# Kernel optimization log

Hardware: AMD Instinct MI355X
Metric: run time of the kernel (lower is better)

The kernel has to match this reference:

```python
import jax, jax.numpy as jnp
import numpy as np

NUM_EMB = 1024
EMB_DIM = 256
COMM_COST = 0.25
BETA = 0.25


def setup_inputs() -> dict:
    key = jax.random.key(0)
    k1, k2 = jax.random.split(key)
    x = jax.random.normal(k1, (16, EMB_DIM, 64, 64), dtype=jnp.float32)
    # nn.Embedding initialized uniform(-1/num_emb, 1/num_emb)
    emb_weight = jax.random.uniform(
        k2, (NUM_EMB, EMB_DIM), dtype=jnp.float32,
        minval=-1.0 / NUM_EMB, maxval=1.0 / NUM_EMB)
    return {"x": x, "emb_weight": emb_weight}


def reference(x, emb_weight):
    # x: [B, C, H, W] -> [B, H, W, C]
    xp = jnp.transpose(x, (0, 2, 3, 1))
    B, H, W, C = xp.shape
    flat = xp.reshape(-1, C)  # [N, C]
    # squared euclidean distances (argmin-equivalent to torch.cdist)
    d2 = (jnp.sum(flat * flat, axis=1, keepdims=True)
          - 2.0 * jnp.einsum('nc,kc->nk', flat, emb_weight)
          + jnp.sum(emb_weight * emb_weight, axis=1))  # [N, K]
    idx = jnp.argmin(d2, axis=1)  # [N]
    quantized = emb_weight[idx].reshape(B, H, W, C)
    e_latent_loss = jnp.mean((jax.lax.stop_gradient(quantized) - xp) ** 2) * BETA
    q_latent_loss = jnp.mean((quantized - jax.lax.stop_gradient(xp)) ** 2)
    c_loss = q_latent_loss + COMM_COST * e_latent_loss
    # straight-through estimator
    quant_st = xp + jax.lax.stop_gradient(quantized - xp)
    quant_out = jnp.transpose(quant_st, (0, 3, 1, 2))  # [B, C, H, W]
    return (c_loss, quant_out)
```

## Files before the change

kernel.cpp:

```cpp
#include <hip/hip_runtime.h>
#include <hip/hip_bf16.h>
#include <cstdint>
#include <cstddef>

#define EMB_K   1024
#define EMB_C   256
#define HWB     4096
#define NPIX    65536

typedef __bf16 bf16x8 __attribute__((ext_vector_type(8)));
typedef float  f32x4  __attribute__((ext_vector_type(4)));

__device__ __forceinline__ unsigned short bf16bits(float v) {
  __hip_bfloat16 h = __float2bfloat16(v);
  return __builtin_bit_cast(unsigned short, h);
}

__global__ void k_emb(const float* __restrict__ emb, unsigned short* __restrict__ emb_bf,
                      float* __restrict__ enorm, float* __restrict__ loss,
                      unsigned* __restrict__ ctr) {
  int k = blockIdx.x;
  int c = threadIdx.x;
  if (k == 0 && c == 0) { *loss = 0.f; *ctr = 0u; }
  float v = emb[(size_t)k * EMB_C + c];
  emb_bf[(size_t)k * EMB_C + c] = bf16bits(v);
  float s = v * v;
  for (int m = 32; m; m >>= 1) s += __shfl_down(s, m, 64);
  __shared__ float red[4];
  int lane = c & 63, w = c >> 6;
  if (lane == 0) red[w] = s;
  __syncthreads();
  if (c == 0) enorm[k] = red[0] + red[1] + red[2] + red[3];
}

__device__ __forceinline__ void stage64(const unsigned short* __restrict__ rows,
                                        unsigned char* buf, int t) {
#pragma unroll
  for (int j = 0; j < 4; ++j) {
    int d = j * 512 + t;
    int r = d >> 5;
    int slot = d & 31;
    int c16 = ((slot >> 3) << 3) | ((slot & 7) ^ (r & 7));
    const unsigned short* src = rows + (size_t)r * EMB_C + c16 * 8;
    __builtin_amdgcn_global_load_lds(
        (const __attribute__((address_space(1))) void*)src,
        (__attribute__((address_space(3))) void*)(buf + (unsigned)(j * 8192 + (t >> 6) * 1024)),
        16, 0, 0);
  }
}

__device__ __forceinline__ int posA(int cc, int nl) {
  return ((cc >> 3) << 3) | ((cc & 7) ^ ((nl ^ (nl >> 2)) & 7));
}

#define LDS_BYTES 137280

__global__ __launch_bounds__(512) void
k_main(const float* __restrict__ x, const float* __restrict__ emb,
       const unsigned short* __restrict__ embbf, const float* __restrict__ enorm,
       float* __restrict__ out, float* __restrict__ loss, unsigned* __restrict__ ctr) {
  extern __shared__ char smem[];
  unsigned char* Abase = (unsigned char*)smem + 65536;
  float*    cjl    = (float*)(smem + 131072);
  unsigned* keys_l = (unsigned*)(smem + 135168);
  float*    xn_l   = (float*)(smem + 136192);
  float*    red    = (float*)(smem + 137216);

  int n0 = blockIdx.x * 256;
  int b  = n0 >> 12, hw0 = n0 & 4095;
  int t = threadIdx.x, w = t >> 6, lane = t & 63;
  int quad = lane >> 4, lr = lane & 15;
  int g  = w >> 1;
  int h2 = w & 1;

  stage64(embbf,               (unsigned char*)smem,         t);
  stage64(embbf + 64 * EMB_C,  (unsigned char*)smem + 32768, t);

  if (t < 256) { keys_l[t] = 0u; xn_l[t] = 0.f; }
  for (int i = t; i < 1024; i += 512) cjl[i] = 0.375f - 0.5f * enorm[i];
  __syncthreads();

  bf16x8 af[4][8];
#pragma unroll
  for (int p = 0; p < 2; ++p) {
    if (p) __syncthreads();
    {
      int hwq = t & 31;
      int cg  = t >> 5;
      const float* xp = x + (size_t)b * (EMB_C * HWB) + hw0 + p * 128 + hwq * 4;
      float xn[4] = {0.f, 0.f, 0.f, 0.f};
      unsigned pk[4][8] = {};
#pragma unroll
      for (int j = 0; j < 16; ++j) {
        f32x4 v = *(const f32x4*)(xp + (size_t)(cg * 16 + j) * HWB);
#pragma unroll
        for (int m = 0; m < 4; ++m) {
          xn[m] += v[m] * v[m];
          pk[m][j >> 1] |= (unsigned)bf16bits(v[m]) << ((j & 1) * 16);
        }
      }
#pragma unroll
      for (int m = 0; m < 4; ++m) {
        int nl = hwq * 4 + m;
        *(uint4*)(Abase + nl * 512 + posA(cg * 2,     nl) * 16) = *(const uint4*)&pk[m][0];
        *(uint4*)(Abase + nl * 512 + posA(cg * 2 + 1, nl) * 16) = *(const uint4*)&pk[m][4];
        atomicAdd(&xn_l[p * 128 + nl], xn[m]);
      }
    }
    __syncthreads();
    if ((g >> 1) == p) {
#pragma unroll
      for (int i = 0; i < 4; ++i) {
        int rA = (g & 1) * 64 + i * 16 + lr;
#pragma unroll
        for (int s = 0; s < 8; ++s) {
          int cc = s * 4 + quad;
          af[i][s] = *(const bf16x8*)(Abase + rA * 512 + posA(cc, rA) * 16);
        }
      }
    }
  }
  __syncthreads();

  unsigned best[4][4] = {};
  for (int kt = 0; kt < 16; ++kt) {
    if (kt < 14)
      stage64(embbf + (size_t)(kt + 2) * 64 * EMB_C,
              (unsigned char*)smem + (((kt + 2) & 3) << 15), t);
    if (kt < 14)       asm volatile("s_waitcnt vmcnt(8)" ::: "memory");
    else if (kt == 14) asm volatile("s_waitcnt vmcnt(4)" ::: "memory");
    else               asm volatile("s_waitcnt vmcnt(0)" ::: "memory");
    __builtin_amdgcn_s_barrier();
    __builtin_amdgcn_sched_barrier(0);
    const unsigned char* srcB = (const unsigned char*)smem + ((kt & 3) << 15);
    float cj[2]; unsigned kp[2];
#pragma unroll
    for (int j = 0; j < 2; ++j) {
      int k = kt * 64 + h2 * 32 + j * 16 + lr;
      cj[j] = cjl[k];
      kp[j] = 1023u - (unsigned)k;
    }
    f32x4 acc[4][2] = {};
#pragma unroll
    for (int s = 0; s < 8; ++s) {
      int cc = s * 4 + quad;
      int pos = ((cc >> 3) << 3) | ((cc & 7) ^ (lr & 7));
      bf16x8 bf[2];
#pragma unroll
      for (int j = 0; j < 2; ++j)
        bf[j] = *(const bf16x8*)(srcB + (h2 * 32 + j * 16 + lr) * 512 + pos * 16);
#pragma unroll
      for (int i = 0; i < 4; ++i)
#pragma unroll
        for (int j = 0; j < 2; ++j)
          acc[i][j] = __builtin_amdgcn_mfma_f32_16x16x32_bf16(af[i][s], bf[j], acc[i][j], 0, 0, 0);
    }
#pragma unroll
    for (int i = 0; i < 4; ++i)
#pragma unroll
      for (int j = 0; j < 2; ++j)
#pragma unroll
        for (int r = 0; r < 4; ++r) {
          float f = acc[i][j][r] + cj[j];
          unsigned key = (__float_as_uint(f) & 0xFFFFFC00u) | kp[j];
          best[i][r] = best[i][r] > key ? best[i][r] : key;
        }
  }
  __syncthreads();

#pragma unroll
  for (int i = 0; i < 4; ++i)
#pragma unroll
    for (int r = 0; r < 4; ++r) {
      unsigned v = best[i][r];
#pragma unroll
      for (int m = 1; m < 16; m <<= 1) {
        unsigned o = (unsigned)__shfl_xor((int)v, m, 64);
        v = v > o ? v : o;
      }
      if (lr == 0) atomicMax(&keys_l[g * 64 + i * 16 + quad * 4 + r], v);
    }
  __syncthreads();

  if (t < 256) {
    unsigned key = keys_l[t];
    float fh = __uint_as_float(key & 0xFFFFFC00u);
    float lsum = xn_l[t] + 0.75f - 2.0f * fh;
    for (int m = 32; m; m >>= 1) lsum += __shfl_down(lsum, m, 64);
    if (lane == 0) red[w] = lsum;
  }
  __syncthreads();
  if (t == 0) {
    atomicAdd(loss, red[0] + red[1] + red[2] + red[3]);
    __threadfence();
  }

  float* tile = (float*)smem;
  int nn = t >> 1, ch = t & 1;
  int idx = 1023 - (int)(keys_l[nn] & 1023u);
  const float* er = emb + (size_t)idx * EMB_C;
  int nrot = (nn - 3) & 255;
  float* ob = out + 1 + (size_t)b * (EMB_C * HWB) + hw0;
  for (int p = 0; p < 4; ++p) {
    int c0 = p * 64;
    if (p) __syncthreads();
#pragma unroll
    for (int q = 0; q < 8; ++q) {
      f32x4 v = *(const f32x4*)(er + c0 + ch * 32 + q * 4);
#pragma unroll
      for (int m = 0; m < 4; ++m)
        tile[(ch * 32 + q * 4 + m) * 256 + nrot] = v[m];
    }
    __syncthreads();
#pragma unroll
    for (int cc = 0; cc < 8; ++cc) {
      int cl = w * 8 + cc;
      const float* tr = tile + cl * 256;
      float* F = ob + (size_t)(c0 + cl) * HWB;
      if (lane < 63) {
        f32x4 q = *(const f32x4*)(tr + 4 * lane);
        *(f32x4*)(F + 3 + 4 * lane) = q;
      }
      if (lane == 0) { F[0] = tr[253]; F[1] = tr[254]; F[2] = tr[255]; }
      if (lane == 63) { F[255] = tr[252]; }
    }
  }

  if (t == 0) {
    unsigned done = atomicAdd(ctr, 1u);
    if (done == gridDim.x - 1) {
      float total = atomicAdd(loss, 0.f);
      out[0] = 1.0625f * total / 16777216.0f;
    }
  }
}

extern "C" void kernel_launch(void* const* d_in, const int* in_sizes, int n_in,
                              void* d_out, int out_size, void* d_ws, size_t ws_size,
                              hipStream_t stream) {
  const float* x   = (const float*)d_in[0];
  const float* emb = (const float*)d_in[1];
  float* out = (float*)d_out;
  char*  ws  = (char*)d_ws;

  unsigned short* emb_bf = (unsigned short*)ws;
  float*          enorm  = (float*)(ws + 524288);
  float*          loss   = (float*)(ws + 528384);
  unsigned*       ctr    = (unsigned*)(ws + 528388);

  hipFuncSetAttribute((const void*)k_main,
                      hipFuncAttributeMaxDynamicSharedMemorySize, LDS_BYTES);

  k_emb <<<dim3(EMB_K),      dim3(EMB_C), 0,         stream>>>(emb, emb_bf, enorm, loss, ctr);
  k_main<<<dim3(NPIX / 256), dim3(512),   LDS_BYTES, stream>>>(x, emb, emb_bf, enorm,
                                                               out, loss, ctr);
}
```

Baseline: 159.4 us.

## Load A fragments directly from global, reshape wave tiling, deepen B prefetch

Each wave now reads its 32 pixels' x values straight from global memory into MFMA A fragments, dropping the LDS transpose round trip, the xn atomics and several barriers. Every wave covers all 64 codes per k-tile on a 32-pixel slice instead of 64 pixels by 32 codes, so the per-pixel argmin no longer needs shared-memory atomicMax. The embedding prefetch becomes three tiles deep and is issued after the barrier. The output gather handles 128 channels per pass with two pixel rows per thread. The trade-off is strided scalar global loads for x in place of coalesced float4 reads, and a different register and LDS balance.

Result: no change. 161.6 us (+1.4%).

```diff
diff --git a/kernel.cpp b/kernel.cpp
--- a/kernel.cpp
+++ b/kernel.cpp
@@ -49,10 +49,6 @@
   }
 }
 
-__device__ __forceinline__ int posA(int cc, int nl) {
-  return ((cc >> 3) << 3) | ((cc & 7) ^ ((nl ^ (nl >> 2)) & 7));
-}
-
 #define LDS_BYTES 137280
 
 __global__ __launch_bounds__(512) void
@@ -60,7 +56,6 @@
        const unsigned short* __restrict__ embbf, const float* __restrict__ enorm,
        float* __restrict__ out, float* __restrict__ loss, unsigned* __restrict__ ctr) {
   extern __shared__ char smem[];
-  unsigned char* Abase = (unsigned char*)smem + 65536;
   float*    cjl    = (float*)(smem + 131072);
   unsigned* keys_l = (unsigned*)(smem + 135168);
   float*    xn_l   = (float*)(smem + 136192);
@@ -70,95 +65,87 @@
   int b  = n0 >> 12, hw0 = n0 & 4095;
   int t = threadIdx.x, w = t >> 6, lane = t & 63;
   int quad = lane >> 4, lr = lane & 15;
-  int g  = w >> 1;
-  int h2 = w & 1;
-
-  stage64(embbf,               (unsigned char*)smem,         t);
-  stage64(embbf + 64 * EMB_C,  (unsigned char*)smem + 32768, t);
-
-  if (t < 256) { keys_l[t] = 0u; xn_l[t] = 0.f; }
+
+  stage64(embbf,                (unsigned char*)smem,          t);
+  stage64(embbf + 64 * EMB_C,   (unsigned char*)smem + 32768,  t);
+  stage64(embbf + 128 * EMB_C,  (unsigned char*)smem + 65536,  t);
+
   for (int i = t; i < 1024; i += 512) cjl[i] = 0.375f - 0.5f * enorm[i];
-  __syncthreads();
-
-  bf16x8 af[4][8];
-#pragma unroll
-  for (int p = 0; p < 2; ++p) {
-    if (p) __syncthreads();
-    {
-      int hwq = t & 31;
-      int cg  = t >> 5;
-      const float* xp = x + (size_t)b * (EMB_C * HWB) + hw0 + p * 128 + hwq * 4;
-      float xn[4] = {0.f, 0.f, 0.f, 0.f};
-      unsigned pk[4][8] = {};
-#pragma unroll
-      for (int j = 0; j < 16; ++j) {
-        f32x4 v = *(const f32x4*)(xp + (size_t)(cg * 16 + j) * HWB);
+
+  bf16x8 af[2][8];
+  float xn2[2];
+  const float* xb = x + (size_t)b * (EMB_C * HWB) + hw0;
+#pragma unroll
+  for (int i = 0; i < 2; ++i) {
+    int rA = w * 32 + i * 16 + lr;
+    float xs = 0.f;
+#pragma unroll
+    for (int s2 = 0; s2 < 4; ++s2) {
+      float v[2][8];
+#pragma unroll
+      for (int h = 0; h < 2; ++h)
+#pragma unroll
+        for (int j = 0; j < 8; ++j)
+          v[h][j] = xb[(size_t)((s2 * 2 + h) * 32 + quad * 8 + j) * HWB + rA];
+#pragma unroll
+      for (int h = 0; h < 2; ++h) {
+        union { unsigned u[4]; bf16x8 f; } pk;
 #pragma unroll
         for (int m = 0; m < 4; ++m) {
-          xn[m] += v[m] * v[m];
-          pk[m][j >> 1] |= (unsigned)bf16bits(v[m]) << ((j & 1) * 16);
+          xs += v[h][2 * m] * v[h][2 * m] + v[h][2 * m + 1] * v[h][2 * m + 1];
+          pk.u[m] = (unsigned)bf16bits(v[h][2 * m]) |
+                    ((unsigned)bf16bits(v[h][2 * m + 1]) << 16);
         }
-      }
-#pragma unroll
-      for (int m = 0; m < 4; ++m) {
-        int nl = hwq * 4 + m;
-        *(uint4*)(Abase + nl * 512 + posA(cg * 2,     nl) * 16) = *(const uint4*)&pk[m][0];
-        *(uint4*)(Abase + nl * 512 + posA(cg * 2 + 1, nl) * 16) = *(const uint4*)&pk[m][4];
-        atomicAdd(&xn_l[p * 128 + nl], xn[m]);
-      }
-    }
-    __syncthreads();
-    if ((g >> 1) == p) {
-#pragma unroll
-      for (int i = 0; i < 4; ++i) {
-        int rA = (g & 1) * 64 + i * 16 + lr;
-#pragma unroll
-        for (int s = 0; s < 8; ++s) {
-          int cc = s * 4 + quad;
-          af[i][s] = *(const bf16x8*)(Abase + rA * 512 + posA(cc, rA) * 16);
-        }
-      }
-    }
-  }
-  __syncthreads();
-
-  unsigned best[4][4] = {};
+        af[i][s2 * 2 + h] = pk.f;
+      }
+    }
+    xn2[i] = xs;
+  }
+#pragma unroll
+  for (int i = 0; i < 2; ++i) {
+    xn2[i] += __shfl_xor(xn2[i], 16, 64);
+    xn2[i] += __shfl_xor(xn2[i], 32, 64);
+  }
+  if (quad == 0) { xn_l[w * 32 + lr] = xn2[0]; xn_l[w * 32 + 16 + lr] = xn2[1]; }
+  __syncthreads();
+
+  unsigned best[2][4] = {};
   for (int kt = 0; kt < 16; ++kt) {
-    if (kt < 14)
-      stage64(embbf + (size_t)(kt + 2) * 64 * EMB_C,
-              (unsigned char*)smem + (((kt + 2) & 3) << 15), t);
     if (kt < 14)       asm volatile("s_waitcnt vmcnt(8)" ::: "memory");
     else if (kt == 14) asm volatile("s_waitcnt vmcnt(4)" ::: "memory");
     else               asm volatile("s_waitcnt vmcnt(0)" ::: "memory");
     __builtin_amdgcn_s_barrier();
     __builtin_amdgcn_sched_barrier(0);
+    if (kt < 13)
+      stage64(embbf + (size_t)(kt + 3) * 64 * EMB_C,
+              (unsigned char*)smem + (((kt + 3) & 3) << 15), t);
     const unsigned char* srcB = (const unsigned char*)smem + ((kt & 3) << 15);
-    float cj[2]; unsigned kp[2];
-#pragma unroll
-    for (int j = 0; j < 2; ++j) {
-      int k = kt * 64 + h2 * 32 + j * 16 + lr;
+    float cj[4]; unsigned kp[4];
+#pragma unroll
+    for (int j = 0; j < 4; ++j) {
+      int k = kt * 64 + j * 16 + lr;
       cj[j] = cjl[k];
       kp[j] = 1023u - (unsigned)k;
     }
-    f32x4 acc[4][2] = {};
+    f32x4 acc[2][4] = {};
 #pragma unroll
     for (int s = 0; s < 8; ++s) {
       int cc = s * 4 + quad;
       int pos = ((cc >> 3) << 3) | ((cc & 7) ^ (lr & 7));
-      bf16x8 bf[2];
-#pragma unroll
-      for (int j = 0; j < 2; ++j)
-        bf[j] = *(const bf16x8*)(srcB + (h2 * 32 + j * 16 + lr) * 512 + pos * 16);
-#pragma unroll
-      for (int i = 0; i < 4; ++i)
-#pragma unroll
-        for (int j = 0; j < 2; ++j)
+      bf16x8 bf[4];
+#pragma unroll
+      for (int j = 0; j < 4; ++j)
+        bf[j] = *(const bf16x8*)(srcB + (j * 16 + lr) * 512 + pos * 16);
+#pragma unroll
+      for (int i = 0; i < 2; ++i)
+#pragma unroll
+        for (int j = 0; j < 4; ++j)
           acc[i][j] = __builtin_amdgcn_mfma_f32_16x16x32_bf16(af[i][s], bf[j], acc[i][j], 0, 0, 0);
     }
 #pragma unroll
-    for (int i = 0; i < 4; ++i)
-#pragma unroll
-      for (int j = 0; j < 2; ++j)
+    for (int i = 0; i < 2; ++i)
+#pragma unroll
+      for (int j = 0; j < 4; ++j)
 #pragma unroll
         for (int r = 0; r < 4; ++r) {
           float f = acc[i][j][r] + cj[j];
@@ -166,10 +153,9 @@
           best[i][r] = best[i][r] > key ? best[i][r] : key;
         }
   }
-  __syncthreads();
-
-#pragma unroll
-  for (int i = 0; i < 4; ++i)
+
+#pragma unroll
+  for (int i = 0; i < 2; ++i)
 #pragma unroll
     for (int r = 0; r < 4; ++r) {
       unsigned v = best[i][r];
@@ -178,7 +164,7 @@
         unsigned o = (unsigned)__shfl_xor((int)v, m, 64);
         v = v > o ? v : o;
       }
-      if (lr == 0) atomicMax(&keys_l[g * 64 + i * 16 + quad * 4 + r], v);
+      if (lr == 0) keys_l[w * 32 + i * 16 + quad * 4 + r] = v;
     }
   __syncthreads();
 
@@ -196,25 +182,31 @@
   }
 
   float* tile = (float*)smem;
-  int nn = t >> 1, ch = t & 1;
-  int idx = 1023 - (int)(keys_l[nn] & 1023u);
-  const float* er = emb + (size_t)idx * EMB_C;
-  int nrot = (nn - 3) & 255;
+  int nn = t >> 2, ch = t & 3;
+  int idxA = 1023 - (int)(keys_l[nn] & 1023u);
+  int idxB = 1023 - (int)(keys_l[128 + nn] & 1023u);
+  const float* erA = emb + (size_t)idxA * EMB_C;
+  const float* erB = emb + (size_t)idxB * EMB_C;
+  int nrotA = (nn - 3) & 255;
+  int nrotB = (nn + 125) & 255;
   float* ob = out + 1 + (size_t)b * (EMB_C * HWB) + hw0;
-  for (int p = 0; p < 4; ++p) {
-    int c0 = p * 64;
+  for (int p = 0; p < 2; ++p) {
+    int c0 = p * 128;
     if (p) __syncthreads();
 #pragma unroll
     for (int q = 0; q < 8; ++q) {
-      f32x4 v = *(const f32x4*)(er + c0 + ch * 32 + q * 4);
-#pragma unroll
-      for (int m = 0; m < 4; ++m)
-        tile[(ch * 32 + q * 4 + m) * 256 + nrot] = v[m];
+      f32x4 va = *(const f32x4*)(erA + c0 + q * 16 + ch * 4);
+      f32x4 vb = *(const f32x4*)(erB + c0 + q * 16 + ch * 4);
+#pragma unroll
+      for (int m = 0; m < 4; ++m) {
+        tile[(q * 16 + ch * 4 + m) * 256 + nrotA] = va[m];
+        tile[(q * 16 + ch * 4 + m) * 256 + nrotB] = vb[m];
+      }
     }
     __syncthreads();
 #pragma unroll
-    for (int cc = 0; cc < 8; ++cc) {
-      int cl = w * 8 + cc;
+    for (int cc = 0; cc < 16; ++cc) {
+      int cl = w * 16 + cc;
       const float* tr = tile + cl * 256;
       float* F = ob + (size_t)(c0 + cl) * HWB;
       if (lane < 63) {
```

## Split codeword gather and output write into a separate kernel

Applied to the files above, without the earlier changes.

The fused epilogue that gathers selected codewords and writes the NCHW output is moved out of the large-LDS main kernel into a new lightweight kernel with many small blocks. The main kernel now only stores argmin keys to global memory and accumulates the loss. The final loss scaling moves to the new kernel, which removes the completion counter. The aim is to run the bandwidth-bound output write at higher occupancy than the 512-thread, 137KB-LDS main kernel allows. The cost is an extra launch and a round trip of the keys through global memory.

Result: no change. 156.9 us (-1.6%).

```diff
diff --git a/kernel.cpp b/kernel.cpp
--- a/kernel.cpp
+++ b/kernel.cpp
@@ -17,11 +17,10 @@
 }
 
 __global__ void k_emb(const float* __restrict__ emb, unsigned short* __restrict__ emb_bf,
-                      float* __restrict__ enorm, float* __restrict__ loss,
-                      unsigned* __restrict__ ctr) {
+                      float* __restrict__ enorm, float* __restrict__ loss) {
   int k = blockIdx.x;
   int c = threadIdx.x;
-  if (k == 0 && c == 0) { *loss = 0.f; *ctr = 0u; }
+  if (k == 0 && c == 0) *loss = 0.f;
   float v = emb[(size_t)k * EMB_C + c];
   emb_bf[(size_t)k * EMB_C + c] = bf16bits(v);
   float s = v * v;
@@ -56,9 +55,9 @@
 #define LDS_BYTES 137280
 
 __global__ __launch_bounds__(512) void
-k_main(const float* __restrict__ x, const float* __restrict__ emb,
-       const unsigned short* __restrict__ embbf, const float* __restrict__ enorm,
-       float* __restrict__ out, float* __restrict__ loss, unsigned* __restrict__ ctr) {
+k_main(const float* __restrict__ x, const unsigned short* __restrict__ embbf,
+       const float* __restrict__ enorm, unsigned* __restrict__ keys_g,
+       float* __restrict__ loss) {
   extern __shared__ char smem[];
   unsigned char* Abase = (unsigned char*)smem + 65536;
   float*    cjl    = (float*)(smem + 131072);
@@ -184,53 +183,48 @@
 
   if (t < 256) {
     unsigned key = keys_l[t];
+    keys_g[n0 + t] = key;
     float fh = __uint_as_float(key & 0xFFFFFC00u);
     float lsum = xn_l[t] + 0.75f - 2.0f * fh;
     for (int m = 32; m; m >>= 1) lsum += __shfl_down(lsum, m, 64);
     if (lane == 0) red[w] = lsum;
   }
   __syncthreads();
-  if (t == 0) {
+  if (t == 0)
     atomicAdd(loss, red[0] + red[1] + red[2] + red[3]);
-    __threadfence();
-  }
-
-  float* tile = (float*)smem;
-  int nn = t >> 1, ch = t & 1;
-  int idx = 1023 - (int)(keys_l[nn] & 1023u);
-  const float* er = emb + (size_t)idx * EMB_C;
-  int nrot = (nn - 3) & 255;
-  float* ob = out + 1 + (size_t)b * (EMB_C * HWB) + hw0;
-  for (int p = 0; p < 4; ++p) {
-    int c0 = p * 64;
+}
+
+__global__ __launch_bounds__(256) void
+k_out(const float* __restrict__ emb, const unsigned* __restrict__ keys_g,
+      const float* __restrict__ loss, float* __restrict__ out) {
+  __shared__ float tile[64 * 65];
+  __shared__ int   idx_l[64];
+  int e  = blockIdx.x;
+  int nt = e >> 1, cH = e & 1;
+  int n0 = nt * 64;
+  int b  = n0 >> 12, hw0 = n0 & 4095;
+  int t = threadIdx.x, w = t >> 6, lane = t & 63;
+  if (e == 0 && t == 0)
+    out[0] = 1.0625f * (*loss) / 16777216.0f;
+  if (t < 64) idx_l[t] = 1023 - (int)(keys_g[n0 + t] & 1023u);
+  __syncthreads();
+  int nn = t >> 2, ch = t & 3;
+  const float* er = emb + (size_t)idx_l[nn] * EMB_C + cH * 128;
+  float* ob = out + 1 + (size_t)b * (EMB_C * HWB) + (size_t)cH * 128 * HWB + hw0;
+  for (int p = 0; p < 2; ++p) {
     if (p) __syncthreads();
 #pragma unroll
-    for (int q = 0; q < 8; ++q) {
-      f32x4 v = *(const f32x4*)(er + c0 + ch * 32 + q * 4);
+    for (int q = 0; q < 4; ++q) {
+      f32x4 v = *(const f32x4*)(er + p * 64 + q * 16 + ch * 4);
 #pragma unroll
       for (int m = 0; m < 4; ++m)
-        tile[(ch * 32 + q * 4 + m) * 256 + nrot] = v[m];
+        tile[(q * 16 + ch * 4 + m) * 65 + nn] = v[m];
     }
     __syncthreads();
 #pragma unroll
-    for (int cc = 0; cc < 8; ++cc) {
-      int cl = w * 8 + cc;
-      const float* tr = tile + cl * 256;
-      float* F = ob + (size_t)(c0 + cl) * HWB;
-      if (lane < 63) {
-        f32x4 q = *(const f32x4*)(tr + 4 * lane);
-        *(f32x4*)(F + 3 + 4 * lane) = q;
-      }
-      if (lane == 0) { F[0] = tr[253]; F[1] = tr[254]; F[2] = tr[255]; }
-      if (lane == 63) { F[255] = tr[252]; }
-    }
-  }
-
-  if (t == 0) {
-    unsigned done = atomicAdd(ctr, 1u);
-    if (done == gridDim.x - 1) {
-      float total = atomicAdd(loss, 0.f);
-      out[0] = 1.0625f * total / 16777216.0f;
+    for (int cc = 0; cc < 16; ++cc) {
+      int cl = w * 16 + cc;
+      ob[(size_t)(p * 64 + cl) * HWB + lane] = tile[cl * 65 + lane];
     }
   }
 }
@@ -246,12 +240,13 @@
   unsigned short* emb_bf = (unsigned short*)ws;
   float*          enorm  = (float*)(ws + 524288);
   float*          loss   = (float*)(ws + 528384);
-  unsigned*       ctr    = (unsigned*)(ws + 528388);
+  unsigned*       keys_g = (unsigned*)(ws + 532480);
 
   hipFuncSetAttribute((const void*)k_main,
                       hipFuncAttributeMaxDynamicSharedMemorySize, LDS_BYTES);
 
-  k_emb <<<dim3(EMB_K),      dim3(EMB_C), 0,         stream>>>(emb, emb_bf, enorm, loss, ctr);
-  k_main<<<dim3(NPIX / 256), dim3(512),   LDS_BYTES, stream>>>(x, emb, emb_bf, enorm,
-                                                               out, loss, ctr);
-}
+  k_emb <<<dim3(EMB_K),      dim3(EMB_C), 0,         stream>>>(emb, emb_bf, enorm, loss);
+  k_main<<<dim3(NPIX / 256), dim3(512),   LDS_BYTES, stream>>>(x, emb_bf, enorm,
+                                                               keys_g, loss);
+  k_out <<<dim3(NPIX / 32),  dim3(256),   0,         stream>>>(emb, keys_g, loss, out);
+}
```
